# Optimization experiments

Hardware: AMD Instinct MI355X
Metric: run time of the kernel (lower is better)

## Reference

```python
import jax, jax.numpy as jnp
import numpy as np

NFRAMES = 8
N_ITERS = 32        # fixed-iteration Riemannian gradient descent (geomstats FrechetMean equivalent)
EPS = 1e-7


def _l2norm(x, axis=-1):
    return x / jnp.maximum(jnp.linalg.norm(x, axis=axis, keepdims=True), EPS)


def _frechet_mean_sphere(X):
    """Batched Frechet mean on the unit hypersphere.
    X: [..., n, d] unit vectors. Returns [..., d] unit mean.
    Iteration: mu <- Exp_mu( mean_i Log_mu(x_i) ).
    """
    mu0 = _l2norm(jnp.mean(X, axis=-2))

    def step(mu, _):
        dots = jnp.clip(jnp.einsum('...d,...kd->...k', mu, X), -1.0 + 1e-6, 1.0 - 1e-6)
        theta = jnp.arccos(dots)
        safe = theta > 1e-4
        coef = jnp.where(safe, theta / jnp.sin(jnp.where(safe, theta, 1.0)), 1.0)
        # Log map: [..., n, d]
        logs = coef[..., None] * (X - dots[..., None] * mu[..., None, :])
        v = jnp.mean(logs, axis=-2)                      # tangent mean [..., d]
        vn = jnp.linalg.norm(v, axis=-1, keepdims=True)
        vsafe = vn > 1e-9
        sinc = jnp.where(vsafe, jnp.sin(vn) / jnp.where(vsafe, vn, 1.0), 1.0)
        mu_new = jnp.cos(vn) * mu + sinc * v             # Exp map
        return _l2norm(mu_new), None

    mu, _ = jax.lax.scan(step, mu0, None, length=N_ITERS)
    return mu


def setup_inputs() -> dict:
    key = jax.random.key(0)
    k1, k2 = jax.random.split(key)
    support_vecs = jax.random.normal(k1, (25, 64, NFRAMES * 2048), dtype=jnp.float32)
    target_vec = jax.random.normal(k2, (64, NFRAMES * 2048), dtype=jnp.float32)
    return {"support_vecs": support_vecs, "target_vec": target_vec}


def reference(support_vecs, target_vec):
    seqlen, bs, df = support_vecs.shape
    sup = _l2norm(support_vecs.reshape(seqlen, bs, NFRAMES, -1))   # [s,b,n,2048]
    tgt = _l2norm(target_vec.reshape(bs, NFRAMES, -1))             # [b,n,2048]
    support_means = _frechet_mean_sphere(sup)                      # [s,b,2048]
    target_means = _frechet_mean_sphere(tgt)                       # [b,2048]
    similarities = jnp.einsum('sbd,bd->sb', support_means, target_means)
    return similarities
```

## Files before the change

kernel.cpp:

```cpp
#include <hip/hip_runtime.h>
#include <math.h>

#define NFR 8
#define DD 2048
#define NS 25
#define NB 64
#define NPAIR (NS*NB)
#define NITER 32

typedef __attribute__((ext_vector_type(8))) short short8;
typedef __attribute__((ext_vector_type(4))) float f32x4;

__device__ __forceinline__ float acos_fast(float x) {
    const float ax = fabsf(x);
    const bool big = ax > 0.5f;
    const float z = big ? 0.5f * (1.f - ax) : x * x;
    const float s = big ? sqrtf(z) : ax;
    float p = fmaf(z, 4.2163199048e-2f, 2.4181311049e-2f);
    p = fmaf(z, p, 4.5470025998e-2f);
    p = fmaf(z, p, 7.4953002686e-2f);
    p = fmaf(z, p, 1.6666752422e-1f);
    const float asin_s = fmaf(s * z, p, s);
    const float asin_abs = big ? (1.5707963267948966f - 2.f * asin_s) : asin_s;
    return 1.5707963267948966f - copysignf(asin_abs, x);
}

__device__ __forceinline__ void split2(float a, float b, unsigned int& hi, unsigned int& lo) {
    unsigned int ua = __float_as_uint(a), ub = __float_as_uint(b);
    unsigned int ha = ua & 0xFFFF0000u, hb = ub & 0xFFFF0000u;
    hi = hb | (ha >> 16);
    float ra = a - __uint_as_float(ha);
    float rb = b - __uint_as_float(hb);
    lo = (__float_as_uint(rb) & 0xFFFF0000u) | (__float_as_uint(ra) >> 16);
}

__global__ __launch_bounds__(256) void fused_kernel(const float* __restrict__ sup,
                                                    const float* __restrict__ tgt,
                                                    float* __restrict__ out) {
    const int p   = blockIdx.x;
    const int tid = threadIdx.x;
    const int wv  = tid >> 6;
    const int l   = tid & 63;
    const int row = l & 15;
    const int kg  = l >> 4;

    __shared__ float part[4][16][17];
    __shared__ float graw[256];

    const float* rowp = (row < 8)
        ? sup + (size_t)p * (NFR*DD) + (size_t)row * DD
        : tgt + (size_t)(p & (NB-1)) * (NFR*DD) + (size_t)(row - 8) * DD;
    const float* ptr = rowp + wv * 512 + kg * 8;

    f32x4 accA = {0.f, 0.f, 0.f, 0.f};
    f32x4 accB = {0.f, 0.f, 0.f, 0.f};
    #pragma unroll 2
    for (int c = 0; c < 16; ++c) {
        float4 f0 = *(const float4*)(ptr);
        float4 f1 = *(const float4*)(ptr + 4);
        ptr += 32;
        union { unsigned int u[4]; short8 s; } H, L;
        split2(f0.x, f0.y, H.u[0], L.u[0]);
        split2(f0.z, f0.w, H.u[1], L.u[1]);
        split2(f1.x, f1.y, H.u[2], L.u[2]);
        split2(f1.z, f1.w, H.u[3], L.u[3]);
        accA = __builtin_amdgcn_mfma_f32_16x16x32_bf16(H.s, H.s, accA, 0, 0, 0);
        accB = __builtin_amdgcn_mfma_f32_16x16x32_bf16(H.s, L.s, accB, 0, 0, 0);
        accB = __builtin_amdgcn_mfma_f32_16x16x32_bf16(L.s, H.s, accB, 0, 0, 0);
    }
    #pragma unroll
    for (int r = 0; r < 4; ++r)
        part[wv][kg * 4 + r][row] = accA[r] + accB[r];
    __syncthreads();

    {
        const int rr = tid >> 4, cc = tid & 15;
        graw[rr * 16 + cc] = part[0][rr][cc] + part[1][rr][cc]
                           + part[2][rr][cc] + part[3][rr][cc];
    }
    __syncthreads();

    if (tid < 16) {
        const int j = tid & 7;
        const int base = tid & 8;
        const int R = base + j;
        const int cb = base;

        const float invn_own = rsqrtf(fmaxf(graw[R * 16 + R], 1e-14f));
        float Grow[8];
        #pragma unroll
        for (int k = 0; k < 8; ++k) {
            const float invk = rsqrtf(fmaxf(graw[(cb + k) * 16 + (cb + k)], 1e-14f));
            Grow[k] = graw[R * 16 + cb + k] * invn_own * invk;
        }

        float rs = 0.f;
        #pragma unroll
        for (int k = 0; k < 8; ++k) rs += Grow[k];
        rs += __shfl_xor(rs, 1, 8);
        rs += __shfl_xor(rs, 2, 8);
        rs += __shfl_xor(rs, 4, 8);
        float a_own = rsqrtf(fmaxf(rs, 6.4e-13f));
        float aAll[8];
        #pragma unroll
        for (int k = 0; k < 8; ++k) aAll[k] = a_own;

        for (int it = 0; it < NITER; ++it) {
            float dot = 0.f;
            #pragma unroll
            for (int k = 0; k < 8; ++k) dot = fmaf(Grow[k], aAll[k], dot);
            dot = fminf(fmaxf(dot, -1.f + 1e-6f), 1.f - 1e-6f);
            const float theta = acos_fast(dot);
            const float q = fmaf(-dot, dot, 1.0f);
            const float coef = (theta > 1e-4f) ? theta * rsqrtf(q) : 1.f;
            const float w = 0.125f * coef;
            float wAll[8];
            #pragma unroll
            for (int k = 0; k < 8; ++k) wAll[k] = __shfl(w, base + k, 16);
            float Gw = 0.f;
            #pragma unroll
            for (int k = 0; k < 8; ++k) Gw = fmaf(Grow[k], wAll[k], Gw);
            float u1 = a_own * Gw, u2 = w * Gw;
            u1 += __shfl_xor(u1, 1, 8);  u2 += __shfl_xor(u2, 1, 8);
            u1 += __shfl_xor(u1, 2, 8);  u2 += __shfl_xor(u2, 2, 8);
            u1 += __shfl_xor(u1, 4, 8);  u2 += __shfl_xor(u2, 4, 8);
            const float cdavg = u1;
            const float vnsq = fmaxf(u2 - cdavg * cdavg, 0.f);
            const float vn = sqrtf(vnsq);
            const float rev = vn * 0.15915494309189535f;
            const float sinv = __builtin_amdgcn_sinf(rev);
            const float cosv = __builtin_amdgcn_cosf(rev);
            const float sinc = (vn > 1e-9f) ? sinv / vn : 1.f;
            const float cn2 = fmaf(sinc * sinc, vnsq, cosv * cosv);
            const float rn = rsqrtf(fmaxf(cn2, 1e-14f));
            a_own = (cosv * a_own + sinc * fmaf(-cdavg, a_own, w)) * rn;
            #pragma unroll
            for (int k = 0; k < 8; ++k)
                aAll[k] = (cosv * aAll[k] + sinc * fmaf(-cdavg, aAll[k], wAll[k])) * rn;
        }

        const float ahat = a_own * invn_own;
        float at[8];
        #pragma unroll
        for (int q2 = 0; q2 < 8; ++q2) at[q2] = __shfl(ahat, 8 + q2, 16);
        float tacc = 0.f;
        #pragma unroll
        for (int q2 = 0; q2 < 8; ++q2) tacc = fmaf(graw[j * 16 + 8 + q2], at[q2], tacc);
        float sim = ahat * tacc;
        sim += __shfl_xor(sim, 1, 8);
        sim += __shfl_xor(sim, 2, 8);
        sim += __shfl_xor(sim, 4, 8);
        if (tid == 0) out[p] = sim;
    }
}

extern "C" void kernel_launch(void* const* d_in, const int* in_sizes, int n_in,
                              void* d_out, int out_size, void* d_ws, size_t ws_size,
                              hipStream_t stream) {
    const float* sup = (const float*)d_in[0];
    const float* tgt = (const float*)d_in[1];
    float* out = (float*)d_out;
    fused_kernel<<<NPAIR, 256, 0, stream>>>(sup, tgt, out);
}
```

Baseline: 50.42 us.

## Split into FP32 Gram kernel with shared target reuse and batched solve kernel

The fused per-pair kernel is replaced by two kernels. The first computes Gram blocks in plain FP32 FMAs: each block covers 5 support sequences for one batch and one K quarter, loading the target slice into LDS once and reusing it. Target self-Grams are computed separately, and partial results go to a workspace. The second kernel sums the partials and runs the 32-iteration sphere solve for 16 pairs per block, so all threads do useful work instead of only 16. This drops the bf16 split MFMA emulation and the redundant target loads, at the cost of a second launch, workspace traffic and heavy register use (100+ accumulators).

New measurement: 99.69 us. +97.7%, slower.

```diff
diff --git a/kernel.cpp b/kernel.cpp
--- a/kernel.cpp
+++ b/kernel.cpp
@@ -7,8 +7,9 @@
 #define NB 64
 #define NPAIR (NS*NB)
 #define NITER 32
-
-typedef __attribute__((ext_vector_type(8))) short short8;
+#define WS_TGT 640000
+#define SOLVE_BLKS 100
+
 typedef __attribute__((ext_vector_type(4))) float f32x4;
 
 __device__ __forceinline__ float acos_fast(float x) {
@@ -25,133 +26,242 @@
     return 1.5707963267948966f - copysignf(asin_abs, x);
 }
 
-__device__ __forceinline__ void split2(float a, float b, unsigned int& hi, unsigned int& lo) {
-    unsigned int ua = __float_as_uint(a), ub = __float_as_uint(b);
-    unsigned int ha = ua & 0xFFFF0000u, hb = ub & 0xFFFF0000u;
-    hi = hb | (ha >> 16);
-    float ra = a - __uint_as_float(ha);
-    float rb = b - __uint_as_float(hb);
-    lo = (__float_as_uint(rb) & 0xFFFF0000u) | (__float_as_uint(ra) >> 16);
-}
-
-__global__ __launch_bounds__(256) void fused_kernel(const float* __restrict__ sup,
-                                                    const float* __restrict__ tgt,
-                                                    float* __restrict__ out) {
-    const int p   = blockIdx.x;
+#define DOT4(acc, A, B) { acc = fmaf(A.x, B.x, acc); acc = fmaf(A.y, B.y, acc); \
+                          acc = fmaf(A.z, B.z, acc); acc = fmaf(A.w, B.w, acc); }
+
+__device__ __forceinline__ void bfly64(float& x) {
+    #pragma unroll
+    for (int m = 1; m <= 32; m <<= 1) x += __shfl_xor(x, m, 64);
+}
+
+__device__ __forceinline__ void load_lds16(const float* g, float* l) {
+    __builtin_amdgcn_global_load_lds(
+        (const __attribute__((address_space(1))) void*)g,
+        (__attribute__((address_space(3))) void*)l, 16, 0, 0);
+}
+
+__global__ __launch_bounds__(320) void gram_kernel(const float* __restrict__ sup,
+                                                   const float* __restrict__ tgt,
+                                                   float* __restrict__ ws) {
+    const int bid = blockIdx.x;
     const int tid = threadIdx.x;
     const int wv  = tid >> 6;
     const int l   = tid & 63;
-    const int row = l & 15;
-    const int kg  = l >> 4;
-
-    __shared__ float part[4][16][17];
-    __shared__ float graw[256];
-
-    const float* rowp = (row < 8)
-        ? sup + (size_t)p * (NFR*DD) + (size_t)row * DD
-        : tgt + (size_t)(p & (NB-1)) * (NFR*DD) + (size_t)(row - 8) * DD;
-    const float* ptr = rowp + wv * 512 + kg * 8;
-
-    f32x4 accA = {0.f, 0.f, 0.f, 0.f};
-    f32x4 accB = {0.f, 0.f, 0.f, 0.f};
-    #pragma unroll 2
-    for (int c = 0; c < 16; ++c) {
-        float4 f0 = *(const float4*)(ptr);
-        float4 f1 = *(const float4*)(ptr + 4);
-        ptr += 32;
-        union { unsigned int u[4]; short8 s; } H, L;
-        split2(f0.x, f0.y, H.u[0], L.u[0]);
-        split2(f0.z, f0.w, H.u[1], L.u[1]);
-        split2(f1.x, f1.y, H.u[2], L.u[2]);
-        split2(f1.z, f1.w, H.u[3], L.u[3]);
-        accA = __builtin_amdgcn_mfma_f32_16x16x32_bf16(H.s, H.s, accA, 0, 0, 0);
-        accB = __builtin_amdgcn_mfma_f32_16x16x32_bf16(H.s, L.s, accB, 0, 0, 0);
-        accB = __builtin_amdgcn_mfma_f32_16x16x32_bf16(L.s, H.s, accB, 0, 0, 0);
-    }
-    #pragma unroll
-    for (int r = 0; r < 4; ++r)
-        part[wv][kg * 4 + r][row] = accA[r] + accB[r];
+
+    __shared__ float tld[8 * 512];
+
+    if (bid < NB) {
+        if (wv < 4) {
+            const int b = bid, kq = wv;
+            const float* tb = tgt + (size_t)b * (NFR*DD) + kq * 512 + l * 4;
+            float4 a0[8], a1[8];
+            #pragma unroll
+            for (int r = 0; r < 8; ++r) a0[r] = *(const float4*)(tb + r * DD);
+            #pragma unroll
+            for (int r = 0; r < 8; ++r) a1[r] = *(const float4*)(tb + r * DD + 256);
+            float tss[36];
+            #pragma unroll
+            for (int i = 0; i < 36; ++i) tss[i] = 0.f;
+            #pragma unroll
+            for (int r1 = 0; r1 < 8; ++r1)
+                #pragma unroll
+                for (int r2 = r1; r2 < 8; ++r2) {
+                    const int i = r1*8 + r2 - r1*(r1+1)/2;
+                    DOT4(tss[i], a0[r1], a0[r2]);
+                    DOT4(tss[i], a1[r1], a1[r2]);
+                }
+            #pragma unroll
+            for (int i = 0; i < 36; ++i) bfly64(tss[i]);
+            if (l == 0) {
+                float4* o4 = (float4*)(ws + WS_TGT + (size_t)(b * 4 + kq) * 36);
+                #pragma unroll
+                for (int i = 0; i < 9; ++i)
+                    o4[i] = make_float4(tss[4*i], tss[4*i+1], tss[4*i+2], tss[4*i+3]);
+            }
+        }
+        return;
+    }
+
+    const int mb = bid - NB;
+    const int b  = mb / 20;
+    const int r20 = mb % 20;
+    const int sq = r20 >> 2;
+    const int kq = r20 & 3;
+    const int s  = sq * 5 + wv;
+    const int p  = s * NB + b;
+
+    for (int seg = wv; seg < 16; seg += 5) {
+        const int r = seg >> 1, h = seg & 1;
+        load_lds16(tgt + ((size_t)b * NFR + r) * DD + kq * 512 + h * 256 + l * 4,
+                   tld + r * 512 + h * 256);
+    }
     __syncthreads();
 
-    {
-        const int rr = tid >> 4, cc = tid & 15;
-        graw[rr * 16 + cc] = part[0][rr][cc] + part[1][rr][cc]
-                           + part[2][rr][cc] + part[3][rr][cc];
+    const float* sb = sup + (size_t)p * (NFR*DD) + kq * 512 + l * 4;
+    float4 sv0[8], sv1[8];
+    #pragma unroll
+    for (int r = 0; r < 8; ++r) sv0[r] = *(const float4*)(sb + r * DD);
+    #pragma unroll
+    for (int r = 0; r < 8; ++r) sv1[r] = *(const float4*)(sb + r * DD + 256);
+
+    float ass[36], ax[64];
+    #pragma unroll
+    for (int i = 0; i < 36; ++i) ass[i] = 0.f;
+    #pragma unroll
+    for (int i = 0; i < 64; ++i) ax[i] = 0.f;
+
+    float4 tv[8];
+    #pragma unroll
+    for (int r = 0; r < 8; ++r) tv[r] = *(const float4*)(tld + r * 512 + l * 4);
+    #pragma unroll
+    for (int r1 = 0; r1 < 8; ++r1)
+        #pragma unroll
+        for (int r2 = r1; r2 < 8; ++r2) {
+            const int i = r1*8 + r2 - r1*(r1+1)/2;
+            DOT4(ass[i], sv0[r1], sv0[r2]);
+        }
+    #pragma unroll
+    for (int r = 0; r < 8; ++r)
+        #pragma unroll
+        for (int t = 0; t < 8; ++t) DOT4(ax[r*8+t], sv0[r], tv[t]);
+
+    #pragma unroll
+    for (int r = 0; r < 8; ++r) tv[r] = *(const float4*)(tld + r * 512 + 256 + l * 4);
+    #pragma unroll
+    for (int r1 = 0; r1 < 8; ++r1)
+        #pragma unroll
+        for (int r2 = r1; r2 < 8; ++r2) {
+            const int i = r1*8 + r2 - r1*(r1+1)/2;
+            DOT4(ass[i], sv1[r1], sv1[r2]);
+        }
+    #pragma unroll
+    for (int r = 0; r < 8; ++r)
+        #pragma unroll
+        for (int t = 0; t < 8; ++t) DOT4(ax[r*8+t], sv1[r], tv[t]);
+
+    #pragma unroll
+    for (int i = 0; i < 36; ++i) bfly64(ass[i]);
+    #pragma unroll
+    for (int i = 0; i < 64; ++i) bfly64(ax[i]);
+
+    if (l == 0) {
+        float4* o4 = (float4*)(ws + (size_t)(p * 4 + kq) * 100);
+        #pragma unroll
+        for (int i = 0; i < 9; ++i)
+            o4[i] = make_float4(ass[4*i], ass[4*i+1], ass[4*i+2], ass[4*i+3]);
+        #pragma unroll
+        for (int i = 0; i < 16; ++i)
+            o4[9+i] = make_float4(ax[4*i], ax[4*i+1], ax[4*i+2], ax[4*i+3]);
+    }
+}
+
+__global__ __launch_bounds__(256) void solve_kernel(const float* __restrict__ ws,
+                                                    float* __restrict__ out) {
+    const int bid = blockIdx.x;
+    const int tid = threadIdx.x;
+    __shared__ float synth[16 * 256];
+
+    for (int e = tid; e < 4096; e += 256) {
+        const int pp = e >> 8, ij = e & 255;
+        const int i = ij >> 4, j = ij & 15;
+        const int p = bid * 16 + pp;
+        const int b = p & (NB - 1);
+        float v = 0.f;
+        if (i < 8) {
+            if (j < 8) {
+                const int ii = i < j ? i : j, jj = i < j ? j : i;
+                const int t36 = ii*8 + jj - ii*(ii+1)/2;
+                #pragma unroll
+                for (int kq = 0; kq < 4; ++kq) v += ws[(size_t)(p*4+kq)*100 + t36];
+            } else {
+                #pragma unroll
+                for (int kq = 0; kq < 4; ++kq) v += ws[(size_t)(p*4+kq)*100 + 36 + i*8 + (j-8)];
+            }
+        } else if (j >= 8) {
+            const int i8 = i - 8, j8 = j - 8;
+            const int ii = i8 < j8 ? i8 : j8, jj = i8 < j8 ? j8 : i8;
+            const int t36 = ii*8 + jj - ii*(ii+1)/2;
+            #pragma unroll
+            for (int kq = 0; kq < 4; ++kq) v += ws[WS_TGT + (size_t)(b*4+kq)*36 + t36];
+        }
+        synth[e] = v;
     }
     __syncthreads();
 
-    if (tid < 16) {
-        const int j = tid & 7;
-        const int base = tid & 8;
-        const int R = base + j;
-        const int cb = base;
-
-        const float invn_own = rsqrtf(fmaxf(graw[R * 16 + R], 1e-14f));
-        float Grow[8];
-        #pragma unroll
-        for (int k = 0; k < 8; ++k) {
-            const float invk = rsqrtf(fmaxf(graw[(cb + k) * 16 + (cb + k)], 1e-14f));
-            Grow[k] = graw[R * 16 + cb + k] * invn_own * invk;
-        }
-
-        float rs = 0.f;
-        #pragma unroll
-        for (int k = 0; k < 8; ++k) rs += Grow[k];
-        rs += __shfl_xor(rs, 1, 8);
-        rs += __shfl_xor(rs, 2, 8);
-        rs += __shfl_xor(rs, 4, 8);
-        float a_own = rsqrtf(fmaxf(rs, 6.4e-13f));
-        float aAll[8];
-        #pragma unroll
-        for (int k = 0; k < 8; ++k) aAll[k] = a_own;
-
-        for (int it = 0; it < NITER; ++it) {
-            float dot = 0.f;
-            #pragma unroll
-            for (int k = 0; k < 8; ++k) dot = fmaf(Grow[k], aAll[k], dot);
-            dot = fminf(fmaxf(dot, -1.f + 1e-6f), 1.f - 1e-6f);
-            const float theta = acos_fast(dot);
-            const float q = fmaf(-dot, dot, 1.0f);
-            const float coef = (theta > 1e-4f) ? theta * rsqrtf(q) : 1.f;
-            const float w = 0.125f * coef;
-            float wAll[8];
-            #pragma unroll
-            for (int k = 0; k < 8; ++k) wAll[k] = __shfl(w, base + k, 16);
-            float Gw = 0.f;
-            #pragma unroll
-            for (int k = 0; k < 8; ++k) Gw = fmaf(Grow[k], wAll[k], Gw);
-            float u1 = a_own * Gw, u2 = w * Gw;
-            u1 += __shfl_xor(u1, 1, 8);  u2 += __shfl_xor(u2, 1, 8);
-            u1 += __shfl_xor(u1, 2, 8);  u2 += __shfl_xor(u2, 2, 8);
-            u1 += __shfl_xor(u1, 4, 8);  u2 += __shfl_xor(u2, 4, 8);
-            const float cdavg = u1;
-            const float vnsq = fmaxf(u2 - cdavg * cdavg, 0.f);
-            const float vn = sqrtf(vnsq);
-            const float rev = vn * 0.15915494309189535f;
-            const float sinv = __builtin_amdgcn_sinf(rev);
-            const float cosv = __builtin_amdgcn_cosf(rev);
-            const float sinc = (vn > 1e-9f) ? sinv / vn : 1.f;
-            const float cn2 = fmaf(sinc * sinc, vnsq, cosv * cosv);
-            const float rn = rsqrtf(fmaxf(cn2, 1e-14f));
-            a_own = (cosv * a_own + sinc * fmaf(-cdavg, a_own, w)) * rn;
-            #pragma unroll
-            for (int k = 0; k < 8; ++k)
-                aAll[k] = (cosv * aAll[k] + sinc * fmaf(-cdavg, aAll[k], wAll[k])) * rn;
-        }
-
-        const float ahat = a_own * invn_own;
-        float at[8];
-        #pragma unroll
-        for (int q2 = 0; q2 < 8; ++q2) at[q2] = __shfl(ahat, 8 + q2, 16);
-        float tacc = 0.f;
-        #pragma unroll
-        for (int q2 = 0; q2 < 8; ++q2) tacc = fmaf(graw[j * 16 + 8 + q2], at[q2], tacc);
-        float sim = ahat * tacc;
-        sim += __shfl_xor(sim, 1, 8);
-        sim += __shfl_xor(sim, 2, 8);
-        sim += __shfl_xor(sim, 4, 8);
-        if (tid == 0) out[p] = sim;
-    }
+    const int pp = tid >> 4;
+    const int t16 = tid & 15;
+    const int p = bid * 16 + pp;
+    const float* graw = synth + pp * 256;
+    const int j = t16 & 7;
+    const int base = t16 & 8;
+    const int R = base + j;
+    const int cb = base;
+
+    const float invn_own = rsqrtf(fmaxf(graw[R * 16 + R], 1e-14f));
+    float Grow[8];
+    #pragma unroll
+    for (int k = 0; k < 8; ++k) {
+        const float invk = rsqrtf(fmaxf(graw[(cb + k) * 16 + (cb + k)], 1e-14f));
+        Grow[k] = graw[R * 16 + cb + k] * invn_own * invk;
+    }
+
+    float rs = 0.f;
+    #pragma unroll
+    for (int k = 0; k < 8; ++k) rs += Grow[k];
+    rs += __shfl_xor(rs, 1, 8);
+    rs += __shfl_xor(rs, 2, 8);
+    rs += __shfl_xor(rs, 4, 8);
+    float a_own = rsqrtf(fmaxf(rs, 6.4e-13f));
+    float aAll[8];
+    #pragma unroll
+    for (int k = 0; k < 8; ++k) aAll[k] = a_own;
+
+    for (int it = 0; it < NITER; ++it) {
+        float dot = 0.f;
+        #pragma unroll
+        for (int k = 0; k < 8; ++k) dot = fmaf(Grow[k], aAll[k], dot);
+        dot = fminf(fmaxf(dot, -1.f + 1e-6f), 1.f - 1e-6f);
+        const float theta = acos_fast(dot);
+        const float q = fmaf(-dot, dot, 1.0f);
+        const float coef = (theta > 1e-4f) ? theta * rsqrtf(q) : 1.f;
+        const float w = 0.125f * coef;
+        float wAll[8];
+        #pragma unroll
+        for (int k = 0; k < 8; ++k) wAll[k] = __shfl(w, base + k, 16);
+        float Gw = 0.f;
+        #pragma unroll
+        for (int k = 0; k < 8; ++k) Gw = fmaf(Grow[k], wAll[k], Gw);
+        float u1 = a_own * Gw, u2 = w * Gw;
+        u1 += __shfl_xor(u1, 1, 8);  u2 += __shfl_xor(u2, 1, 8);
+        u1 += __shfl_xor(u1, 2, 8);  u2 += __shfl_xor(u2, 2, 8);
+        u1 += __shfl_xor(u1, 4, 8);  u2 += __shfl_xor(u2, 4, 8);
+        const float cdavg = u1;
+        const float vnsq = fmaxf(u2 - cdavg * cdavg, 0.f);
+        const float vn = sqrtf(vnsq);
+        const float rev = vn * 0.15915494309189535f;
+        const float sinv = __builtin_amdgcn_sinf(rev);
+        const float cosv = __builtin_amdgcn_cosf(rev);
+        const float sinc = (vn > 1e-9f) ? sinv / vn : 1.f;
+        const float cn2 = fmaf(sinc * sinc, vnsq, cosv * cosv);
+        const float rn = rsqrtf(fmaxf(cn2, 1e-14f));
+        a_own = (cosv * a_own + sinc * fmaf(-cdavg, a_own, w)) * rn;
+        #pragma unroll
+        for (int k = 0; k < 8; ++k)
+            aAll[k] = (cosv * aAll[k] + sinc * fmaf(-cdavg, aAll[k], wAll[k])) * rn;
+    }
+
+    const float ahat = a_own * invn_own;
+    float at[8];
+    #pragma unroll
+    for (int q2 = 0; q2 < 8; ++q2) at[q2] = __shfl(ahat, 8 + q2, 16);
+    float tacc = 0.f;
+    #pragma unroll
+    for (int q2 = 0; q2 < 8; ++q2) tacc = fmaf(graw[j * 16 + 8 + q2], at[q2], tacc);
+    float sim = ahat * tacc;
+    sim += __shfl_xor(sim, 1, 8);
+    sim += __shfl_xor(sim, 2, 8);
+    sim += __shfl_xor(sim, 4, 8);
+    if (t16 == 0) out[p] = sim;
 }
 
 extern "C" void kernel_launch(void* const* d_in, const int* in_sizes, int n_in,
@@ -159,6 +269,8 @@
                               hipStream_t stream) {
     const float* sup = (const float*)d_in[0];
     const float* tgt = (const float*)d_in[1];
+    float* ws = (float*)d_ws;
     float* out = (float*)d_out;
-    fused_kernel<<<NPAIR, 256, 0, stream>>>(sup, tgt, out);
-}
+    gram_kernel<<<NB + NB * 20, 320, 0, stream>>>(sup, tgt, ws);
+    solve_kernel<<<SOLVE_BLKS, 256, 0, stream>>>(ws, out);
+}
```
